# Optimization experiments

Hardware: AMD Instinct MI355X
Metric: run time of the kernel (lower is better)

Reference implementation:

```python
import jax, jax.numpy as jnp
import numpy as np

# Module hyperparameters (from init_kwargs)
NBITS = 8
FOLD = 8
B = 8192
IN_F = 2048
OUT_F = 2048
ISIZE = IN_F // FOLD   # 256
OSIZE = OUT_F // FOLD  # 256
QMAX = 2 ** (NBITS - 1) - 1  # 127


def setup_inputs() -> dict:
    key = jax.random.key(0)
    k1, k2, k3, k4, k5 = jax.random.split(key, 5)
    inp = jax.random.normal(k1, (B, IN_F), dtype=jnp.float32)
    # per-fold linear weights, torch nn.Linear default-ish scale
    W = jax.random.normal(k2, (FOLD, OSIZE, ISIZE), dtype=jnp.float32) * (1.0 / np.sqrt(ISIZE))
    # UniformPositionalEncoding buffers: offset + per-fold per-column ranges
    pe = jax.random.normal(k3, (1, FOLD, ISIZE), dtype=jnp.float32) * 0.1
    min_range = -jax.random.uniform(k4, (1, FOLD, ISIZE), minval=0.25, maxval=1.0, dtype=jnp.float32)
    max_range = jax.random.uniform(k5, (1, FOLD, ISIZE), minval=0.25, maxval=1.0, dtype=jnp.float32)
    return {"input": inp, "W": W, "pe": pe, "min_range": min_range, "max_range": max_range}


def reference(input, W, pe, min_range, max_range):
    b = input.shape[0]
    x = input.reshape(b, FOLD, ISIZE)
    # QuantAct symmetric, clamp_only=True: per-tensor scale s = max|x| / n, clamp to [-s*n, s*n]
    s = jnp.max(jnp.abs(x)) / QMAX
    x = jnp.clip(x, -s * QMAX, s * QMAX)
    s = s * QMAX  # scaled range multiplier
    # positional offset, broadcast over batch
    x = x + pe[0]  # [b, FOLD, ISIZE]
    x_flat = x.reshape(b * FOLD, ISIZE)

    def per_fold(Wi, mn, mx):
        # fold_idx_ste forward passes full x through; range mask zeroes out-of-range entries
        mask = (x_flat < mn * s) | (x_flat > mx * s)  # [b*FOLD, ISIZE]
        xm = jnp.where(mask, jnp.float32(0.0), x_flat)
        o = xm @ Wi.T  # [b*FOLD, OSIZE]
        return o.reshape(b, FOLD, OSIZE).sum(axis=1)  # [b, OSIZE]

    # vmap over the FOLD small linears
    out = jax.vmap(per_fold)(W, min_range[0], max_range[0])  # [FOLD, b, OSIZE]
    out = jnp.transpose(out, (1, 0, 2)).reshape(b, FOLD * OSIZE)  # stack dim=1 then flatten
    return out
```

## Files before the change

### kernel.cpp

```cpp
#include <hip/hip_runtime.h>

#define FOLD  8
#define ISIZE 256
#define IN_F  2048
#define OUT_F 2048

#define TBM2  16
#define NBLK2 (8192 / TBM2)
#define CHW2  560

#define TBM   32
#define NBLK  (8192 / TBM)
#define CHW   1104

typedef __attribute__((ext_vector_type(8))) short short8;
typedef __attribute__((ext_vector_type(4))) float f32x4;

__device__ __forceinline__ unsigned f2bf(float f) {
    unsigned u = __float_as_uint(f);
    u += 0x7FFFu + ((u >> 16) & 1u);
    return (u >> 16);
}

__global__ __launch_bounds__(256)
void absmax_conv(const float4* __restrict__ in,
                 const float* __restrict__ W,
                 float* __restrict__ partials,
                 unsigned short* __restrict__ wsw,
                 int quota) {
    const int nthreads = gridDim.x * 256;
    const int idx = blockIdx.x * 256 + threadIdx.x;

    if (blockIdx.x < 256) {
        const int t    = blockIdx.x * 256 + threadIdx.x;
        const int wid  = t >> 6;
        const int l    = t & 63;
        const int i  = wid >> 7;
        const int nt = (wid >> 3) & 15;
        const int ks = wid & 7;
        const int n = l & 15, q = l >> 4;
        const float* src = W + (((size_t)i * 256 + nt * 16 + n) * 256 + ks * 32 + q * 8);
        float4 s0 = *(const float4*)(src);
        float4 s1 = *(const float4*)(src + 4);
        uint4 p;
        p.x = f2bf(s0.x) | (f2bf(s0.y) << 16);
        p.y = f2bf(s0.z) | (f2bf(s0.w) << 16);
        p.z = f2bf(s1.x) | (f2bf(s1.y) << 16);
        p.w = f2bf(s1.z) | (f2bf(s1.w) << 16);
        *(uint4*)(wsw + (size_t)wid * 512 + l * 8) = p;
    }

    float m = 0.f;
    #pragma unroll 4
    for (int q = 0; q < quota; ++q) {
        float4 a = in[idx + q * nthreads];
        m = fmaxf(m, fmaxf(fmaxf(fabsf(a.x), fabsf(a.y)),
                           fmaxf(fabsf(a.z), fabsf(a.w))));
    }
    #pragma unroll
    for (int off = 32; off > 0; off >>= 1)
        m = fmaxf(m, __shfl_down(m, off, 64));
    __shared__ float sm[4];
    int lane = threadIdx.x & 63, wv = threadIdx.x >> 6;
    if (lane == 0) sm[wv] = m;
    __syncthreads();
    if (threadIdx.x == 0)
        partials[blockIdx.x] = fmaxf(fmaxf(sm[0], sm[1]), fmaxf(sm[2], sm[3]));
}

__global__ __launch_bounds__(256)
void absmax_kernel(const float4* __restrict__ in,
                   float* __restrict__ partials,
                   unsigned int* __restrict__ scal,
                   int quota, int mode) {
    const int nthreads = gridDim.x * 256;
    const int idx = blockIdx.x * 256 + threadIdx.x;
    float m = 0.f;
    #pragma unroll 4
    for (int q = 0; q < quota; ++q) {
        float4 a = in[idx + q * nthreads];
        m = fmaxf(m, fmaxf(fmaxf(fabsf(a.x), fabsf(a.y)),
                           fmaxf(fabsf(a.z), fabsf(a.w))));
    }
    #pragma unroll
    for (int off = 32; off > 0; off >>= 1)
        m = fmaxf(m, __shfl_down(m, off, 64));
    __shared__ float sm[4];
    int lane = threadIdx.x & 63, wv = threadIdx.x >> 6;
    if (lane == 0) sm[wv] = m;
    __syncthreads();
    if (threadIdx.x == 0) {
        float r = fmaxf(fmaxf(sm[0], sm[1]), fmaxf(sm[2], sm[3]));
        if (mode) partials[blockIdx.x] = r;
        else      atomicMax(scal, __float_as_uint(r));
    }
}

__global__ __launch_bounds__(512, 4)
void fold2(const float* __restrict__ in,
           const unsigned short* __restrict__ wsw,
           const float* __restrict__ pe,
           const float* __restrict__ mn,
           const float* __restrict__ mx,
           const float* __restrict__ partials,
           int npart,
           float* __restrict__ out) {
    __shared__ __align__(16) unsigned short ylds[64 * CHW2];
    __shared__ float sred[8];

    const int tid  = threadIdx.x;
    const int lane = tid & 63;
    const int wv   = tid >> 6;
    const int row0 = blockIdx.x * TBM2;

    float mabs;
    {
        float v = 0.f;
        for (int p = tid; p < npart; p += 512) v = fmaxf(v, partials[p]);
        #pragma unroll
        for (int off = 32; off > 0; off >>= 1)
            v = fmaxf(v, __shfl_down(v, off, 64));
        if (lane == 0) sred[wv] = v;
        __syncthreads();
        float r = sred[0];
        #pragma unroll
        for (int i = 1; i < 8; ++i) r = fmaxf(r, sred[i]);
        mabs = r;
    }
    const float c = (mabs / 127.0f) * 127.0f;

    {
        const int kp  = tid & 127;
        const int rq  = tid >> 7;
        const int k0  = kp * 2;
        const int jh  = kp & 3;
        const int qA  = (kp >> 2) & 3;
        const int ksA = kp >> 4;

        float pef[FOLD][2], lo[FOLD][2], hi[FOLD][2];
        #pragma unroll
        for (int f = 0; f < FOLD; ++f) {
            float2 p2 = *(const float2*)(pe + f * ISIZE + k0);
            pef[f][0] = p2.x; pef[f][1] = p2.y;
        }
        #pragma unroll
        for (int i = 0; i < FOLD; ++i) {
            float2 a2 = *(const float2*)(mn + i * ISIZE + k0);
            float2 b2 = *(const float2*)(mx + i * ISIZE + k0);
            lo[i][0] = a2.x * c; lo[i][1] = a2.y * c;
            hi[i][0] = b2.x * c; hi[i][1] = b2.y * c;
        }

        #pragma unroll
        for (int r4 = 0; r4 < 4; ++r4) {
            const int row = rq * 4 + r4;
            const float* rowp = in + (size_t)(row0 + row) * IN_F + k0;
            float2 xr[FOLD];
            #pragma unroll
            for (int f = 0; f < FOLD; ++f) xr[f] = *(const float2*)(rowp + f * ISIZE);

            float acc[FOLD][2];
            #pragma unroll
            for (int i = 0; i < FOLD; ++i) { acc[i][0] = 0.0f; acc[i][1] = 0.0f; }
            #pragma unroll
            for (int f = 0; f < FOLD; ++f) {
                float xv0 = fminf(fmaxf(xr[f].x, -c), c) + pef[f][0];
                float xv1 = fminf(fmaxf(xr[f].y, -c), c) + pef[f][1];
                #pragma unroll
                for (int i = 0; i < FOLD; ++i) {
                    if (xv0 >= lo[i][0] && xv0 <= hi[i][0]) acc[i][0] += xv0;
                    if (xv1 >= lo[i][1] && xv1 <= hi[i][1]) acc[i][1] += xv1;
                }
            }
            const unsigned base = (unsigned)(qA * 136 + row * 8 + jh * 2);
            #pragma unroll
            for (int i = 0; i < FOLD; ++i) {
                unsigned us = f2bf(acc[i][0]) | (f2bf(acc[i][1]) << 16);
                *(unsigned*)&ylds[(i * 8 + ksA) * CHW2 + base] = us;
            }
        }
    }
    __syncthreads();

    {
        const int fi   = wv;
        const int mrow = lane & 15;
        const int quad = lane >> 4;

        short8 afr[8];
        #pragma unroll
        for (int kk = 0; kk < 8; ++kk)
            afr[kk] = *(const short8*)&ylds[(fi * 8 + kk) * CHW2 + quad * 136 + mrow * 8];

        const int col0 = fi * 256 + mrow;
        #pragma unroll 2
        for (int ntg = 0; ntg < 16; ++ntg) {
            f32x4 a0 = (f32x4){0.f, 0.f, 0.f, 0.f};
            const unsigned short* wb = wsw + ((size_t)(fi * 16 + ntg) * 8) * 512 + lane * 8;
            uint4 wq[8];
            #pragma unroll
            for (int kk = 0; kk < 8; ++kk) wq[kk] = *(const uint4*)(wb + kk * 512);
            #pragma unroll
            for (int kk = 0; kk < 8; ++kk) {
                union { uint4 u; short8 s; } cv; cv.u = wq[kk];
                a0 = __builtin_amdgcn_mfma_f32_16x16x32_bf16(afr[kk], cv.s, a0, 0, 0, 0);
            }
            #pragma unroll
            for (int rg = 0; rg < 4; ++rg)
                out[(size_t)(row0 + quad * 4 + rg) * OUT_F + col0 + ntg * 16] = a0[rg];
        }
    }
}

__global__ __launch_bounds__(1024, 1)
void fold_main(const float* __restrict__ in,
               const float* __restrict__ W,
               const float* __restrict__ pe,
               const float* __restrict__ mn,
               const float* __restrict__ mx,
               const float* __restrict__ partials,
               const unsigned int* __restrict__ scal,
               int npart,
               float* __restrict__ out) {
    __shared__ __align__(16) unsigned short ylds[64 * CHW];
    __shared__ float sred[16];

    const int tid  = threadIdx.x;
    const int lane = tid & 63;
    const int wv   = tid >> 6;
    const int row0 = blockIdx.x * TBM;

    float mabs;
    if (npart > 0) {
        float v = (tid < npart) ? partials[tid] : 0.0f;
        #pragma unroll
        for (int off = 32; off > 0; off >>= 1)
            v = fmaxf(v, __shfl_down(v, off, 64));
        if (lane == 0) sred[wv] = v;
        __syncthreads();
        float r = sred[0];
        #pragma unroll
        for (int i = 1; i < 16; ++i) r = fmaxf(r, sred[i]);
        mabs = r;
    } else {
        mabs = __uint_as_float(*scal);
    }
    const float c = (mabs / 127.0f) * 127.0f;

    {
        const int kp  = tid & 127;
        const int rq  = tid >> 7;
        const int k0  = kp * 2;
        const int jh  = kp & 3;
        const int qA  = (kp >> 2) & 3;
        const int ksA = kp >> 4;

        float pef[FOLD][2], lo[FOLD][2], hi[FOLD][2];
        #pragma unroll
        for (int f = 0; f < FOLD; ++f) {
            float2 p2 = *(const float2*)(pe + f * ISIZE + k0);
            pef[f][0] = p2.x; pef[f][1] = p2.y;
        }
        #pragma unroll
        for (int i = 0; i < FOLD; ++i) {
            float2 a2 = *(const float2*)(mn + i * ISIZE + k0);
            float2 b2 = *(const float2*)(mx + i * ISIZE + k0);
            lo[i][0] = a2.x * c; lo[i][1] = a2.y * c;
            hi[i][0] = b2.x * c; hi[i][1] = b2.y * c;
        }

        #pragma unroll
        for (int r4 = 0; r4 < 4; ++r4) {
            const int row = rq * 4 + r4;
            const float* rowp = in + (size_t)(row0 + row) * IN_F + k0;
            float2 xr[FOLD];
            #pragma unroll
            for (int f = 0; f < FOLD; ++f) xr[f] = *(const float2*)(rowp + f * ISIZE);

            float acc[FOLD][2];
            #pragma unroll
            for (int i = 0; i < FOLD; ++i) { acc[i][0] = 0.0f; acc[i][1] = 0.0f; }
            #pragma unroll
            for (int f = 0; f < FOLD; ++f) {
                float xv0 = fminf(fmaxf(xr[f].x, -c), c) + pef[f][0];
                float xv1 = fminf(fmaxf(xr[f].y, -c), c) + pef[f][1];
                #pragma unroll
                for (int i = 0; i < FOLD; ++i) {
                    if (xv0 >= lo[i][0] && xv0 <= hi[i][0]) acc[i][0] += xv0;
                    if (xv1 >= lo[i][1] && xv1 <= hi[i][1]) acc[i][1] += xv1;
                }
            }
            const unsigned base = (unsigned)((row >> 4) * 544 + qA * 136 + (row & 15) * 8 + jh * 2);
            #pragma unroll
            for (int i = 0; i < FOLD; ++i) {
                unsigned us = f2bf(acc[i][0]) | (f2bf(acc[i][1]) << 16);
                *(unsigned*)&ylds[(i * 8 + ksA) * CHW + base] = us;
            }
        }
    }
    __syncthreads();

    {
        const int fi   = wv >> 1;
        const int nh   = wv & 1;
        const int mrow = lane & 15;
        const int quad = lane >> 4;

        short8 afr[8][2];
        #pragma unroll
        for (int kk = 0; kk < 8; ++kk) {
            #pragma unroll
            for (int mt = 0; mt < 2; ++mt)
                afr[kk][mt] = *(const short8*)&ylds[(fi * 8 + kk) * CHW + mt * 544 + quad * 136 + mrow * 8];
        }

        const int col0 = fi * 256 + mrow;
        #pragma unroll 2
        for (int nt8 = 0; nt8 < 8; ++nt8) {
            const int ntg = nh * 8 + nt8;
            f32x4 a0 = (f32x4){0.f, 0.f, 0.f, 0.f};
            f32x4 a1 = (f32x4){0.f, 0.f, 0.f, 0.f};
            const float* wb = W + ((size_t)(fi * 256 + ntg * 16 + mrow) * 256 + quad * 8);
            float4 w[16];
            #pragma unroll
            for (int kk = 0; kk < 8; ++kk) {
                w[2 * kk]     = *(const float4*)(wb + kk * 32);
                w[2 * kk + 1] = *(const float4*)(wb + kk * 32 + 4);
            }
            #pragma unroll
            for (int kk = 0; kk < 8; ++kk) {
                union { uint4 u; short8 s; } cv;
                cv.u.x = f2bf(w[2*kk].x)   | (f2bf(w[2*kk].y)   << 16);
                cv.u.y = f2bf(w[2*kk].z)   | (f2bf(w[2*kk].w)   << 16);
                cv.u.z = f2bf(w[2*kk+1].x) | (f2bf(w[2*kk+1].y) << 16);
                cv.u.w = f2bf(w[2*kk+1].z) | (f2bf(w[2*kk+1].w) << 16);
                a0 = __builtin_amdgcn_mfma_f32_16x16x32_bf16(afr[kk][0], cv.s, a0, 0, 0, 0);
                a1 = __builtin_amdgcn_mfma_f32_16x16x32_bf16(afr[kk][1], cv.s, a1, 0, 0, 0);
            }
            #pragma unroll
            for (int rg = 0; rg < 4; ++rg) {
                out[(size_t)(row0 +      quad * 4 + rg) * OUT_F + col0 + ntg * 16] = a0[rg];
                out[(size_t)(row0 + 16 + quad * 4 + rg) * OUT_F + col0 + ntg * 16] = a1[rg];
            }
        }
    }
}

extern "C" void kernel_launch(void* const* d_in, const int* in_sizes, int n_in,
                              void* d_out, int out_size, void* d_ws, size_t ws_size,
                              hipStream_t stream) {
    const float* in = (const float*)d_in[0];
    const float* W  = (const float*)d_in[1];
    const float* pe = (const float*)d_in[2];
    const float* mn = (const float*)d_in[3];
    const float* mx = (const float*)d_in[4];
    float* out = (float*)d_out;

    const size_t PART_OFF  = 16;
    const size_t WSW_OFF   = 8192;
    const size_t WSW_BYTES = (size_t)FOLD * 256 * 256 * 2;

    unsigned int*   scal     = (unsigned int*)d_ws;
    float*          partials = (float*)((char*)d_ws + PART_OFF);
    unsigned short* wsw      = (unsigned short*)((char*)d_ws + WSW_OFF);

    const bool preconv = ws_size >= WSW_OFF + WSW_BYTES;

    if (preconv && ws_size >= PART_OFF + 1024 * sizeof(float)) {
        absmax_conv<<<1024, 256, 0, stream>>>((const float4*)in, W, partials, wsw, 16);
        fold2<<<NBLK2, 512, 0, stream>>>(in, wsw, pe, mn, mx, partials, 1024, out);
        return;
    }

    int npart;
    if (ws_size >= PART_OFF + 1024 * sizeof(float)) {
        absmax_kernel<<<1024, 256, 0, stream>>>((const float4*)in, partials, scal, 16, 1);
        npart = 1024;
    } else if (ws_size >= PART_OFF + 256 * sizeof(float)) {
        absmax_kernel<<<256, 256, 0, stream>>>((const float4*)in, partials, scal, 64, 1);
        npart = 256;
    } else {
        hipMemsetAsync(d_ws, 0, sizeof(unsigned int), stream);
        absmax_kernel<<<256, 256, 0, stream>>>((const float4*)in, partials, scal, 64, 0);
        npart = 0;
    }
    fold_main<<<NBLK, 1024, 0, stream>>>(in, W, pe, mn, mx,
                                         partials, scal, npart, out);
}
```

Measured before the change: 150.8 us.

## Use 32-row 1024-thread tiles with nontemporal loads and stores

Replaces the 16-row, 512-thread fold kernel with a 32-row, 1024-thread version. Each wave handles two M-tiles over half the N range, so every weight fragment loaded from global memory feeds two MFMAs. Input reads in both kernels and output writes now use nontemporal loads and stores to reduce cache pollution. The cost is one block per CU with a larger LDS footprint, which lowers occupancy and the ability to hide latency.

Measured after the change: 155.1 us. +2.9%, slower.

```diff
diff --git a/kernel.cpp b/kernel.cpp
--- a/kernel.cpp
+++ b/kernel.cpp
@@ -4,17 +4,13 @@
 #define ISIZE 256
 #define IN_F  2048
 #define OUT_F 2048
-
-#define TBM2  16
-#define NBLK2 (8192 / TBM2)
-#define CHW2  560
-
 #define TBM   32
 #define NBLK  (8192 / TBM)
 #define CHW   1104
 
 typedef __attribute__((ext_vector_type(8))) short short8;
 typedef __attribute__((ext_vector_type(4))) float f32x4;
+typedef __attribute__((ext_vector_type(2))) float f32x2;
 
 __device__ __forceinline__ unsigned f2bf(float f) {
     unsigned u = __float_as_uint(f);
@@ -23,7 +19,7 @@
 }
 
 __global__ __launch_bounds__(256)
-void absmax_conv(const float4* __restrict__ in,
+void absmax_conv(const float* __restrict__ in,
                  const float* __restrict__ W,
                  float* __restrict__ partials,
                  unsigned short* __restrict__ wsw,
@@ -53,9 +49,10 @@
     float m = 0.f;
     #pragma unroll 4
     for (int q = 0; q < quota; ++q) {
-        float4 a = in[idx + q * nthreads];
-        m = fmaxf(m, fmaxf(fmaxf(fabsf(a.x), fabsf(a.y)),
-                           fmaxf(fabsf(a.z), fabsf(a.w))));
+        f32x4 a = __builtin_nontemporal_load(
+            (const f32x4*)(in + (size_t)(idx + q * nthreads) * 4));
+        m = fmaxf(m, fmaxf(fmaxf(fabsf(a[0]), fabsf(a[1])),
+                           fmaxf(fabsf(a[2]), fabsf(a[3]))));
     }
     #pragma unroll
     for (int off = 32; off > 0; off >>= 1)
@@ -96,27 +93,26 @@
     }
 }
 
-__global__ __launch_bounds__(512, 4)
-void fold2(const float* __restrict__ in,
-           const unsigned short* __restrict__ wsw,
-           const float* __restrict__ pe,
-           const float* __restrict__ mn,
-           const float* __restrict__ mx,
-           const float* __restrict__ partials,
-           int npart,
-           float* __restrict__ out) {
-    __shared__ __align__(16) unsigned short ylds[64 * CHW2];
-    __shared__ float sred[8];
+__global__ __launch_bounds__(1024, 1)
+void fold_nt(const float* __restrict__ in,
+             const unsigned short* __restrict__ wsw,
+             const float* __restrict__ pe,
+             const float* __restrict__ mn,
+             const float* __restrict__ mx,
+             const float* __restrict__ partials,
+             int npart,
+             float* __restrict__ out) {
+    __shared__ __align__(16) unsigned short ylds[64 * CHW];
+    __shared__ float sred[16];
 
     const int tid  = threadIdx.x;
     const int lane = tid & 63;
     const int wv   = tid >> 6;
-    const int row0 = blockIdx.x * TBM2;
+    const int row0 = blockIdx.x * TBM;
 
     float mabs;
     {
-        float v = 0.f;
-        for (int p = tid; p < npart; p += 512) v = fmaxf(v, partials[p]);
+        float v = (tid < npart) ? partials[tid] : 0.0f;
         #pragma unroll
         for (int off = 32; off > 0; off >>= 1)
             v = fmaxf(v, __shfl_down(v, off, 64));
@@ -124,7 +120,7 @@
         __syncthreads();
         float r = sred[0];
         #pragma unroll
-        for (int i = 1; i < 8; ++i) r = fmaxf(r, sred[i]);
+        for (int i = 1; i < 16; ++i) r = fmaxf(r, sred[i]);
         mabs = r;
     }
     const float c = (mabs / 127.0f) * 127.0f;
@@ -155,47 +151,54 @@
         for (int r4 = 0; r4 < 4; ++r4) {
             const int row = rq * 4 + r4;
             const float* rowp = in + (size_t)(row0 + row) * IN_F + k0;
-            float2 xr[FOLD];
-            #pragma unroll
-            for (int f = 0; f < FOLD; ++f) xr[f] = *(const float2*)(rowp + f * ISIZE);
+            f32x2 xr[FOLD];
+            #pragma unroll
+            for (int f = 0; f < FOLD; ++f)
+                xr[f] = __builtin_nontemporal_load((const f32x2*)(rowp + f * ISIZE));
 
             float acc[FOLD][2];
             #pragma unroll
             for (int i = 0; i < FOLD; ++i) { acc[i][0] = 0.0f; acc[i][1] = 0.0f; }
             #pragma unroll
             for (int f = 0; f < FOLD; ++f) {
-                float xv0 = fminf(fmaxf(xr[f].x, -c), c) + pef[f][0];
-                float xv1 = fminf(fmaxf(xr[f].y, -c), c) + pef[f][1];
+                float xv0 = fminf(fmaxf(xr[f][0], -c), c) + pef[f][0];
+                float xv1 = fminf(fmaxf(xr[f][1], -c), c) + pef[f][1];
                 #pragma unroll
                 for (int i = 0; i < FOLD; ++i) {
                     if (xv0 >= lo[i][0] && xv0 <= hi[i][0]) acc[i][0] += xv0;
                     if (xv1 >= lo[i][1] && xv1 <= hi[i][1]) acc[i][1] += xv1;
                 }
             }
-            const unsigned base = (unsigned)(qA * 136 + row * 8 + jh * 2);
+            const unsigned base = (unsigned)((row >> 4) * 544 + qA * 136 + (row & 15) * 8 + jh * 2);
             #pragma unroll
             for (int i = 0; i < FOLD; ++i) {
                 unsigned us = f2bf(acc[i][0]) | (f2bf(acc[i][1]) << 16);
-                *(unsigned*)&ylds[(i * 8 + ksA) * CHW2 + base] = us;
+                *(unsigned*)&ylds[(i * 8 + ksA) * CHW + base] = us;
             }
         }
     }
     __syncthreads();
 
     {
-        const int fi   = wv;
+        const int fi   = wv >> 1;
+        const int nh   = wv & 1;
         const int mrow = lane & 15;
         const int quad = lane >> 4;
 
-        short8 afr[8];
-        #pragma unroll
-        for (int kk = 0; kk < 8; ++kk)
-            afr[kk] = *(const short8*)&ylds[(fi * 8 + kk) * CHW2 + quad * 136 + mrow * 8];
+        short8 afr[8][2];
+        #pragma unroll
+        for (int kk = 0; kk < 8; ++kk) {
+            #pragma unroll
+            for (int mt = 0; mt < 2; ++mt)
+                afr[kk][mt] = *(const short8*)&ylds[(fi * 8 + kk) * CHW + mt * 544 + quad * 136 + mrow * 8];
+        }
 
         const int col0 = fi * 256 + mrow;
         #pragma unroll 2
-        for (int ntg = 0; ntg < 16; ++ntg) {
+        for (int nt8 = 0; nt8 < 8; ++nt8) {
+            const int ntg = nh * 8 + nt8;
             f32x4 a0 = (f32x4){0.f, 0.f, 0.f, 0.f};
+            f32x4 a1 = (f32x4){0.f, 0.f, 0.f, 0.f};
             const unsigned short* wb = wsw + ((size_t)(fi * 16 + ntg) * 8) * 512 + lane * 8;
             uint4 wq[8];
             #pragma unroll
@@ -203,11 +206,16 @@
             #pragma unroll
             for (int kk = 0; kk < 8; ++kk) {
                 union { uint4 u; short8 s; } cv; cv.u = wq[kk];
-                a0 = __builtin_amdgcn_mfma_f32_16x16x32_bf16(afr[kk], cv.s, a0, 0, 0, 0);
-            }
-            #pragma unroll
-            for (int rg = 0; rg < 4; ++rg)
-                out[(size_t)(row0 + quad * 4 + rg) * OUT_F + col0 + ntg * 16] = a0[rg];
+                a0 = __builtin_amdgcn_mfma_f32_16x16x32_bf16(afr[kk][0], cv.s, a0, 0, 0, 0);
+                a1 = __builtin_amdgcn_mfma_f32_16x16x32_bf16(afr[kk][1], cv.s, a1, 0, 0, 0);
+            }
+            #pragma unroll
+            for (int rg = 0; rg < 4; ++rg) {
+                __builtin_nontemporal_store(a0[rg],
+                    &out[(size_t)(row0 +      quad * 4 + rg) * OUT_F + col0 + ntg * 16]);
+                __builtin_nontemporal_store(a1[rg],
+                    &out[(size_t)(row0 + 16 + quad * 4 + rg) * OUT_F + col0 + ntg * 16]);
+            }
         }
     }
 }
@@ -367,8 +375,8 @@
     const bool preconv = ws_size >= WSW_OFF + WSW_BYTES;
 
     if (preconv && ws_size >= PART_OFF + 1024 * sizeof(float)) {
-        absmax_conv<<<1024, 256, 0, stream>>>((const float4*)in, W, partials, wsw, 16);
-        fold2<<<NBLK2, 512, 0, stream>>>(in, wsw, pe, mn, mx, partials, 1024, out);
+        absmax_conv<<<1024, 256, 0, stream>>>(in, W, partials, wsw, 16);
+        fold_nt<<<NBLK, 1024, 0, stream>>>(in, wsw, pe, mn, mx, partials, 1024, out);
         return;
     }
 
@@ -380,7 +388,7 @@
         absmax_kernel<<<256, 256, 0, stream>>>((const float4*)in, partials, scal, 64, 1);
         npart = 256;
     } else {
-        hipMemsetAsync(d_ws, 0, sizeof(unsigned int), stream);
+        (void)hipMemsetAsync(d_ws, 0, sizeof(unsigned int), stream);
         absmax_kernel<<<256, 256, 0, stream>>>((const float4*)in, partials, scal, 64, 0);
         npart = 0;
     }
```
